# Kernel optimization log

Measured on AMD Instinct MI355X. Metric: run time of the kernel, lower is better.

## Reference

```python
import jax, jax.numpy as jnp
import numpy as np

# EXP-HYDRO concrete realization of HydrologyModel.
# Parameter order matches _parameter_bounds key order; bounds per standard EXP-HYDRO.
PARAM_BOUNDS = [
    ("f",    0.0,  0.1),
    ("Smax", 100.0, 1500.0),
    ("Qmax", 10.0, 50.0),
    ("Df",   0.0,  5.0),
    ("Tmax", 0.0,  3.0),
    ("Tmin", -3.0, 0.0),
]
NEARZERO = 1e-6
T_STEPS = 1024
N_BASINS = 8192
N_PARAMS = len(PARAM_BOUNDS)


def _denormalize(static_params_norm):
    # sigmoid activation then affine map to bounds; returns dict name -> [B]
    act = jax.nn.sigmoid(static_params_norm)  # [B, P]
    return {name: lo + (hi - lo) * act[:, i]
            for i, (name, lo, hi) in enumerate(PARAM_BOUNDS)}


def _run_core(prcp, temp, pet, params, nearzero=NEARZERO):
    # prcp/temp/pet: [T, B]; params: dict of [B]
    f, Smax, Qmax = params["f"], params["Smax"], params["Qmax"]
    Df, Tmax, Tmin = params["Df"], params["Tmax"], params["Tmin"]

    def step(states, forc_t):
        snowpack, soilwater = states
        prcp_t, temp_t, pet_t = forc_t
        # hydroflux formulas (elementwise over basins)
        snowfall = jnp.where(temp_t < Tmin, prcp_t, 0.0)
        rainfall = prcp_t - snowfall
        melt = jnp.minimum(snowpack, Df * jnp.maximum(temp_t - Tmax, 0.0))
        evap = pet_t * jnp.minimum(soilwater / Smax, 1.0)
        baseflow = Qmax * jnp.exp(-f * jnp.maximum(Smax - soilwater, 0.0))
        surfaceflow = jnp.maximum(soilwater - Smax, 0.0)
        # stateflux formulas (state changes)
        d_snow = snowfall - melt
        d_soil = rainfall + melt - evap - baseflow - surfaceflow
        # state update with clamp(min=nearzero)
        new_snow = jnp.maximum(snowpack + d_snow, nearzero)
        new_soil = jnp.maximum(soilwater + d_soil, nearzero)
        out = jnp.stack([snowfall, rainfall, melt, evap,
                         baseflow, surfaceflow, d_snow, d_soil])  # [8, B]
        return (new_snow, new_soil), out

    B = prcp.shape[1]
    init = (jnp.zeros((B,), prcp.dtype), jnp.zeros((B,), prcp.dtype))
    _, outs = jax.lax.scan(step, init, (prcp, temp, pet))
    return outs  # [T, 8, B]


def setup_inputs() -> dict:
    key = jax.random.key(0)
    k1, k2, k3, k4 = jax.random.split(key, 4)
    prcp = jax.random.uniform(k1, (T_STEPS, N_BASINS), jnp.float32) * 10.0  # mm/day
    temp = jax.random.normal(k2, (T_STEPS, N_BASINS), jnp.float32) * 5.0    # deg C
    pet = jax.random.uniform(k3, (T_STEPS, N_BASINS), jnp.float32) * 5.0    # mm/day
    static_params_norm = jax.random.normal(k4, (N_BASINS, N_PARAMS), jnp.float32)
    return {"prcp": prcp, "temp": temp, "pet": pet,
            "static_params_norm": static_params_norm}


def reference(prcp, temp, pet, static_params_norm):
    params = _denormalize(static_params_norm)
    return _run_core(prcp, temp, pet, params)  # [T, 8, B]
```

## Files before the change

kernel.cpp:

```cpp
#include <hip/hip_runtime.h>

#define T_STEPS 1024
#define NB 8192
#define OUT_TSTRIDE (8 * NB)

__device__ __forceinline__ float sigmoidf_(float x) {
    return 1.0f / (1.0f + __expf(-x));
}

#define STEP(PR, TM, PE, TI)                                                   \
    do {                                                                       \
        float snowfall    = ((TM) < Tmin) ? (PR) : 0.0f;                       \
        float rainfall    = (PR) - snowfall;                                   \
        float melt        = fminf(snow, Df * fmaxf((TM) - Tmax, 0.0f));        \
        float evap        = (PE) * fminf(soil * rSmax, 1.0f);                  \
        float baseflow    = Qmax * __expf(nf * fmaxf(Smax - soil, 0.0f));      \
        float surfaceflow = fmaxf(soil - Smax, 0.0f);                          \
        float d_snow      = snowfall - melt;                                   \
        float d_soil = (((rainfall + melt) - evap) - baseflow) - surfaceflow;  \
        snow = fmaxf(snow + d_snow, 1e-6f);                                    \
        soil = fmaxf(soil + d_soil, 1e-6f);                                    \
        float sv;                                                              \
        if (CH == 0)      sv = snowfall;                                       \
        else if (CH == 1) sv = rainfall;                                       \
        else if (CH == 2) sv = melt;                                           \
        else if (CH == 3) sv = evap;                                           \
        else if (CH == 4) sv = baseflow;                                       \
        else if (CH == 5) sv = surfaceflow;                                    \
        else if (CH == 6) sv = d_snow;                                         \
        else              sv = d_soil;                                         \
        op[(size_t)(TI) * OUT_TSTRIDE] = sv;                                   \
    } while (0)

template <int CH>
__device__ __forceinline__ void run_basin(const float* __restrict__ pp,
                                          const float* __restrict__ tp,
                                          const float* __restrict__ ep,
                                          float* __restrict__ op, float f,
                                          float Smax, float Qmax, float Df,
                                          float Tmax, float Tmin) {
    const float rSmax = 1.0f / Smax;
    const float nf    = -f;
    float snow = 0.0f, soil = 0.0f;

    float Pa[8], Ta[8], Ea[8], Pb[8], Tb[8], Eb[8];
#pragma unroll
    for (int i = 0; i < 8; ++i) {
        Pa[i] = pp[i * NB];
        Ta[i] = tp[i * NB];
        Ea[i] = ep[i * NB];
    }
#pragma unroll
    for (int i = 0; i < 8; ++i) {
        Pb[i] = pp[(8 + i) * NB];
        Tb[i] = tp[(8 + i) * NB];
        Eb[i] = ep[(8 + i) * NB];
    }

    for (int tb = 0; tb < T_STEPS; tb += 16) {
#pragma unroll
        for (int i = 0; i < 8; ++i) STEP(Pa[i], Ta[i], Ea[i], tb + i);
#pragma unroll
        for (int i = 0; i < 8; ++i) {
            int t2 = tb + 16 + i;
            t2     = (t2 > T_STEPS - 1) ? (T_STEPS - 1) : t2;
            Pa[i]  = pp[t2 * NB];
            Ta[i]  = tp[t2 * NB];
            Ea[i]  = ep[t2 * NB];
        }
#pragma unroll
        for (int i = 0; i < 8; ++i) STEP(Pb[i], Tb[i], Eb[i], tb + 8 + i);
#pragma unroll
        for (int i = 0; i < 8; ++i) {
            int t2 = tb + 24 + i;
            t2     = (t2 > T_STEPS - 1) ? (T_STEPS - 1) : t2;
            Pb[i]  = pp[t2 * NB];
            Tb[i]  = tp[t2 * NB];
            Eb[i]  = ep[t2 * NB];
        }
    }
}

extern "C" __global__ void __launch_bounds__(256, 1)
    hydro_kernel(const float* __restrict__ prcp, const float* __restrict__ temp,
                 const float* __restrict__ pet, const float* __restrict__ spn,
                 float* __restrict__ out) {
    const int lane  = threadIdx.x & 63;
    const int wav   = threadIdx.x >> 6;
    const int h     = blockIdx.x & 1;
    const int g     = blockIdx.x >> 1;
    const int basin = g * 64 + lane;
    const int ch    = h * 4 + wav;

    const float* p6  = spn + basin * 6;
    const float f    = 0.1f * sigmoidf_(p6[0]);
    const float Smax = 100.0f + 1400.0f * sigmoidf_(p6[1]);
    const float Qmax = 10.0f + 40.0f * sigmoidf_(p6[2]);
    const float Df   = 5.0f * sigmoidf_(p6[3]);
    const float Tmax = 3.0f * sigmoidf_(p6[4]);
    const float Tmin = -3.0f + 3.0f * sigmoidf_(p6[5]);

    const float* pp = prcp + basin;
    const float* tp = temp + basin;
    const float* ep = pet + basin;
    float* op       = out + (size_t)ch * NB + basin;

    switch (__builtin_amdgcn_readfirstlane(ch)) {
        case 0: run_basin<0>(pp, tp, ep, op, f, Smax, Qmax, Df, Tmax, Tmin); break;
        case 1: run_basin<1>(pp, tp, ep, op, f, Smax, Qmax, Df, Tmax, Tmin); break;
        case 2: run_basin<2>(pp, tp, ep, op, f, Smax, Qmax, Df, Tmax, Tmin); break;
        case 3: run_basin<3>(pp, tp, ep, op, f, Smax, Qmax, Df, Tmax, Tmin); break;
        case 4: run_basin<4>(pp, tp, ep, op, f, Smax, Qmax, Df, Tmax, Tmin); break;
        case 5: run_basin<5>(pp, tp, ep, op, f, Smax, Qmax, Df, Tmax, Tmin); break;
        case 6: run_basin<6>(pp, tp, ep, op, f, Smax, Qmax, Df, Tmax, Tmin); break;
        default: run_basin<7>(pp, tp, ep, op, f, Smax, Qmax, Df, Tmax, Tmin); break;
    }
}

extern "C" void kernel_launch(void* const* d_in, const int* in_sizes, int n_in,
                              void* d_out, int out_size, void* d_ws,
                              size_t ws_size, hipStream_t stream) {
    const float* prcp = (const float*)d_in[0];
    const float* temp = (const float*)d_in[1];
    const float* pet  = (const float*)d_in[2];
    const float* spn  = (const float*)d_in[3];
    float* out        = (float*)d_out;

    hydro_kernel<<<dim3(256), dim3(256), 0, stream>>>(prcp, temp, pet, spn, out);
}
```

Baseline: 405.9 us.

## Split time into segments with prefix recompute and two channels per wave

Each wave now stores two output channels instead of one, halving the redundant recurrence evaluation per basin. The time axis is split into four 256-step segments across more blocks, and each block replays the prefix of the recurrence without stores to rebuild its starting state. This increases the number of resident blocks and cuts total arithmetic, at the cost of uneven per-block work and larger register arrays for deeper prefetch.

Result: slower. 435.2 us (+7.2%).

```diff
diff --git a/kernel.cpp b/kernel.cpp
--- a/kernel.cpp
+++ b/kernel.cpp
@@ -8,89 +8,124 @@
     return 1.0f / (1.0f + __expf(-x));
 }
 
-#define STEP(PR, TM, PE, TI)                                                   \
+#define CORE(PR, TM, PE)                                                       \
+    float snowfall    = ((TM) < Tmin) ? (PR) : 0.0f;                           \
+    float rainfall    = (PR) - snowfall;                                       \
+    float melt        = fminf(snow, Df * fmaxf((TM) - Tmax, 0.0f));            \
+    float evap        = (PE) * fminf(soil * rSmax, 1.0f);                      \
+    float baseflow    = Qmax * __expf(nf * fmaxf(Smax - soil, 0.0f));          \
+    float surfaceflow = fmaxf(soil - Smax, 0.0f);                              \
+    float d_snow      = snowfall - melt;                                       \
+    float d_soil = (((rainfall + melt) - evap) - baseflow) - surfaceflow;      \
+    snow = fmaxf(snow + d_snow, 1e-6f);                                        \
+    soil = fmaxf(soil + d_soil, 1e-6f);
+
+#define STEP_NS(PR, TM, PE)                                                    \
     do {                                                                       \
-        float snowfall    = ((TM) < Tmin) ? (PR) : 0.0f;                       \
-        float rainfall    = (PR) - snowfall;                                   \
-        float melt        = fminf(snow, Df * fmaxf((TM) - Tmax, 0.0f));        \
-        float evap        = (PE) * fminf(soil * rSmax, 1.0f);                  \
-        float baseflow    = Qmax * __expf(nf * fmaxf(Smax - soil, 0.0f));      \
-        float surfaceflow = fmaxf(soil - Smax, 0.0f);                          \
-        float d_snow      = snowfall - melt;                                   \
-        float d_soil = (((rainfall + melt) - evap) - baseflow) - surfaceflow;  \
-        snow = fmaxf(snow + d_snow, 1e-6f);                                    \
-        soil = fmaxf(soil + d_soil, 1e-6f);                                    \
-        float sv;                                                              \
-        if (CH == 0)      sv = snowfall;                                       \
-        else if (CH == 1) sv = rainfall;                                       \
-        else if (CH == 2) sv = melt;                                           \
-        else if (CH == 3) sv = evap;                                           \
-        else if (CH == 4) sv = baseflow;                                       \
-        else if (CH == 5) sv = surfaceflow;                                    \
-        else if (CH == 6) sv = d_snow;                                         \
-        else              sv = d_soil;                                         \
-        op[(size_t)(TI) * OUT_TSTRIDE] = sv;                                   \
+        CORE(PR, TM, PE)                                                       \
+        (void)rainfall; (void)evap; (void)baseflow; (void)surfaceflow;         \
+        (void)d_snow; (void)d_soil;                                            \
     } while (0)
 
-template <int CH>
+#define STEP_ST(PR, TM, PE)                                                    \
+    do {                                                                       \
+        CORE(PR, TM, PE)                                                       \
+        float sv0, sv1;                                                        \
+        if (CP == 0)      { sv0 = snowfall; sv1 = rainfall; }                  \
+        else if (CP == 1) { sv0 = melt;     sv1 = evap; }                      \
+        else if (CP == 2) { sv0 = baseflow; sv1 = surfaceflow; }               \
+        else              { sv0 = d_snow;   sv1 = d_soil; }                    \
+        op[0]  = sv0;                                                          \
+        op[NB] = sv1;                                                          \
+        op += OUT_TSTRIDE;                                                     \
+    } while (0)
+
+template <int CP>
 __device__ __forceinline__ void run_basin(const float* __restrict__ pp,
                                           const float* __restrict__ tp,
                                           const float* __restrict__ ep,
                                           float* __restrict__ op, float f,
                                           float Smax, float Qmax, float Df,
-                                          float Tmax, float Tmin) {
+                                          float Tmax, float Tmin,
+                                          int segStart) {
     const float rSmax = 1.0f / Smax;
     const float nf    = -f;
     float snow = 0.0f, soil = 0.0f;
 
-    float Pa[8], Ta[8], Ea[8], Pb[8], Tb[8], Eb[8];
+    float Pa[16], Ta[16], Ea[16], Pb[16], Tb[16], Eb[16];
+
+    if (segStart > 0) {
 #pragma unroll
-    for (int i = 0; i < 8; ++i) {
-        Pa[i] = pp[i * NB];
-        Ta[i] = tp[i * NB];
-        Ea[i] = ep[i * NB];
+        for (int i = 0; i < 16; ++i) {
+            Pa[i] = pp[i * NB]; Ta[i] = tp[i * NB]; Ea[i] = ep[i * NB];
+        }
+#pragma unroll
+        for (int i = 0; i < 16; ++i) {
+            Pb[i] = pp[(16 + i) * NB]; Tb[i] = tp[(16 + i) * NB];
+            Eb[i] = ep[(16 + i) * NB];
+        }
+        for (int tb = 0; tb < segStart; tb += 32) {
+#pragma unroll
+            for (int i = 0; i < 16; ++i) STEP_NS(Pa[i], Ta[i], Ea[i]);
+#pragma unroll
+            for (int i = 0; i < 16; ++i) {
+                int t2 = tb + 32 + i;
+                Pa[i] = pp[t2 * NB]; Ta[i] = tp[t2 * NB]; Ea[i] = ep[t2 * NB];
+            }
+#pragma unroll
+            for (int i = 0; i < 16; ++i) STEP_NS(Pb[i], Tb[i], Eb[i]);
+#pragma unroll
+            for (int i = 0; i < 16; ++i) {
+                int t2 = tb + 48 + i;
+                Pb[i] = pp[t2 * NB]; Tb[i] = tp[t2 * NB]; Eb[i] = ep[t2 * NB];
+            }
+        }
+    }
+
+#pragma unroll
+    for (int i = 0; i < 16; ++i) {
+        int t = segStart + i;
+        Pa[i] = pp[t * NB]; Ta[i] = tp[t * NB]; Ea[i] = ep[t * NB];
     }
 #pragma unroll
-    for (int i = 0; i < 8; ++i) {
-        Pb[i] = pp[(8 + i) * NB];
-        Tb[i] = tp[(8 + i) * NB];
-        Eb[i] = ep[(8 + i) * NB];
+    for (int i = 0; i < 16; ++i) {
+        int t = segStart + 16 + i;
+        Pb[i] = pp[t * NB]; Tb[i] = tp[t * NB]; Eb[i] = ep[t * NB];
     }
-
-    for (int tb = 0; tb < T_STEPS; tb += 16) {
+    for (int tb = segStart; tb < segStart + 256; tb += 32) {
 #pragma unroll
-        for (int i = 0; i < 8; ++i) STEP(Pa[i], Ta[i], Ea[i], tb + i);
+        for (int i = 0; i < 16; ++i) STEP_ST(Pa[i], Ta[i], Ea[i]);
 #pragma unroll
-        for (int i = 0; i < 8; ++i) {
-            int t2 = tb + 16 + i;
-            t2     = (t2 > T_STEPS - 1) ? (T_STEPS - 1) : t2;
-            Pa[i]  = pp[t2 * NB];
-            Ta[i]  = tp[t2 * NB];
-            Ea[i]  = ep[t2 * NB];
+        for (int i = 0; i < 16; ++i) {
+            int t2 = tb + 32 + i;
+            t2 = (t2 > T_STEPS - 1) ? (T_STEPS - 1) : t2;
+            Pa[i] = pp[t2 * NB]; Ta[i] = tp[t2 * NB]; Ea[i] = ep[t2 * NB];
         }
 #pragma unroll
-        for (int i = 0; i < 8; ++i) STEP(Pb[i], Tb[i], Eb[i], tb + 8 + i);
+        for (int i = 0; i < 16; ++i) STEP_ST(Pb[i], Tb[i], Eb[i]);
 #pragma unroll
-        for (int i = 0; i < 8; ++i) {
-            int t2 = tb + 24 + i;
-            t2     = (t2 > T_STEPS - 1) ? (T_STEPS - 1) : t2;
-            Pb[i]  = pp[t2 * NB];
-            Tb[i]  = tp[t2 * NB];
-            Eb[i]  = ep[t2 * NB];
+        for (int i = 0; i < 16; ++i) {
+            int t2 = tb + 48 + i;
+            t2 = (t2 > T_STEPS - 1) ? (T_STEPS - 1) : t2;
+            Pb[i] = pp[t2 * NB]; Tb[i] = tp[t2 * NB]; Eb[i] = ep[t2 * NB];
         }
     }
 }
 
-extern "C" __global__ void __launch_bounds__(256, 1)
+extern "C" __global__ void __launch_bounds__(256, 2)
     hydro_kernel(const float* __restrict__ prcp, const float* __restrict__ temp,
                  const float* __restrict__ pet, const float* __restrict__ spn,
                  float* __restrict__ out) {
     const int lane  = threadIdx.x & 63;
-    const int wav   = threadIdx.x >> 6;
-    const int h     = blockIdx.x & 1;
-    const int g     = blockIdx.x >> 1;
-    const int basin = g * 64 + lane;
-    const int ch    = h * 4 + wav;
+    const int w     = threadIdx.x >> 6;
+    const int b     = blockIdx.x;
+    const int x     = b & 7;
+    const int r     = b >> 3;
+    const int seg   = r & 3;
+    const int gg    = r >> 2;
+    const int group = gg * 8 + x;
+    const int basin = group * 64 + lane;
+    const int segStart = seg << 8;
 
     const float* p6  = spn + basin * 6;
     const float f    = 0.1f * sigmoidf_(p6[0]);
@@ -103,17 +138,13 @@
     const float* pp = prcp + basin;
     const float* tp = temp + basin;
     const float* ep = pet + basin;
-    float* op       = out + (size_t)ch * NB + basin;
+    float* op = out + (size_t)segStart * OUT_TSTRIDE + (size_t)(2 * w) * NB + basin;
 
-    switch (__builtin_amdgcn_readfirstlane(ch)) {
-        case 0: run_basin<0>(pp, tp, ep, op, f, Smax, Qmax, Df, Tmax, Tmin); break;
-        case 1: run_basin<1>(pp, tp, ep, op, f, Smax, Qmax, Df, Tmax, Tmin); break;
-        case 2: run_basin<2>(pp, tp, ep, op, f, Smax, Qmax, Df, Tmax, Tmin); break;
-        case 3: run_basin<3>(pp, tp, ep, op, f, Smax, Qmax, Df, Tmax, Tmin); break;
-        case 4: run_basin<4>(pp, tp, ep, op, f, Smax, Qmax, Df, Tmax, Tmin); break;
-        case 5: run_basin<5>(pp, tp, ep, op, f, Smax, Qmax, Df, Tmax, Tmin); break;
-        case 6: run_basin<6>(pp, tp, ep, op, f, Smax, Qmax, Df, Tmax, Tmin); break;
-        default: run_basin<7>(pp, tp, ep, op, f, Smax, Qmax, Df, Tmax, Tmin); break;
+    switch (__builtin_amdgcn_readfirstlane(w)) {
+        case 0:  run_basin<0>(pp, tp, ep, op, f, Smax, Qmax, Df, Tmax, Tmin, segStart); break;
+        case 1:  run_basin<1>(pp, tp, ep, op, f, Smax, Qmax, Df, Tmax, Tmin, segStart); break;
+        case 2:  run_basin<2>(pp, tp, ep, op, f, Smax, Qmax, Df, Tmax, Tmin, segStart); break;
+        default: run_basin<3>(pp, tp, ep, op, f, Smax, Qmax, Df, Tmax, Tmin, segStart); break;
     }
 }
 
@@ -126,5 +157,5 @@
     const float* spn  = (const float*)d_in[3];
     float* out        = (float*)d_out;
 
-    hydro_kernel<<<dim3(256), dim3(256), 0, stream>>>(prcp, temp, pet, spn, out);
+    hydro_kernel<<<dim3(512), dim3(256), 0, stream>>>(prcp, temp, pet, spn, out);
 }
```

## Stage forcings in LDS via async loads, two channels per wave, split store ranges

Applied to the files above, without the earlier changes.

Forcing tiles of 32 timesteps are copied into double-buffered LDS with global_load_lds, so the four waves of a block share one load instead of each reading global memory separately. Each wave now emits two output channels instead of one. Two block types are paired per basin group: both run the recurrence from the start, and each stores a different range of output tiles so store work is split evenly. The cost is redundant recurrence computation, since one block type re-runs 24 to 32 tiles, plus a block-wide barrier on every tile.

New measurement: 372.5 us. 1.09x faster.

```diff
diff --git a/kernel.cpp b/kernel.cpp
--- a/kernel.cpp
+++ b/kernel.cpp
@@ -1,83 +1,89 @@
 #include <hip/hip_runtime.h>
+#include <stdint.h>
 
-#define T_STEPS 1024
 #define NB 8192
 #define OUT_TSTRIDE (8 * NB)
+#define TILE 32
+#define LDS_F 6144
 
 __device__ __forceinline__ float sigmoidf_(float x) {
     return 1.0f / (1.0f + __expf(-x));
 }
 
-#define STEP(PR, TM, PE, TI)                                                   \
-    do {                                                                       \
-        float snowfall    = ((TM) < Tmin) ? (PR) : 0.0f;                       \
-        float rainfall    = (PR) - snowfall;                                   \
-        float melt        = fminf(snow, Df * fmaxf((TM) - Tmax, 0.0f));        \
-        float evap        = (PE) * fminf(soil * rSmax, 1.0f);                  \
-        float baseflow    = Qmax * __expf(nf * fmaxf(Smax - soil, 0.0f));      \
-        float surfaceflow = fmaxf(soil - Smax, 0.0f);                          \
-        float d_snow      = snowfall - melt;                                   \
-        float d_soil = (((rainfall + melt) - evap) - baseflow) - surfaceflow;  \
-        snow = fmaxf(snow + d_snow, 1e-6f);                                    \
-        soil = fmaxf(soil + d_soil, 1e-6f);                                    \
-        float sv;                                                              \
-        if (CH == 0)      sv = snowfall;                                       \
-        else if (CH == 1) sv = rainfall;                                       \
-        else if (CH == 2) sv = melt;                                           \
-        else if (CH == 3) sv = evap;                                           \
-        else if (CH == 4) sv = baseflow;                                       \
-        else if (CH == 5) sv = surfaceflow;                                    \
-        else if (CH == 6) sv = d_snow;                                         \
-        else              sv = d_soil;                                         \
-        op[(size_t)(TI) * OUT_TSTRIDE] = sv;                                   \
-    } while (0)
+__device__ __forceinline__ void async16(const float* g, float* l) {
+    __builtin_amdgcn_global_load_lds(
+        (const __attribute__((address_space(1))) void*)g,
+        (__attribute__((address_space(3))) void*)l, 16, 0, 0);
+}
 
-template <int CH>
-__device__ __forceinline__ void run_basin(const float* __restrict__ pp,
-                                          const float* __restrict__ tp,
-                                          const float* __restrict__ ep,
-                                          float* __restrict__ op, float f,
-                                          float Smax, float Qmax, float Df,
-                                          float Tmax, float Tmin) {
+__device__ __forceinline__ void fill_tile(const float* __restrict__ prcp,
+                                          const float* __restrict__ temp,
+                                          const float* __restrict__ pet,
+                                          float* lds, int t0, int tid,
+                                          int gbase) {
+#pragma unroll
+    for (int r = 0; r < 6; ++r) {
+        const float* src = (r < 2) ? prcp : ((r < 4) ? temp : pet);
+        int tt = ((r & 1) << 4) + (tid >> 4);
+        int t  = t0 + tt;
+        t      = (t > 1023) ? 1023 : t;
+        const float* g = src + (size_t)t * NB + gbase + ((tid & 15) << 2);
+        float* l       = lds + (r << 10) + (tid << 2);
+        async16(g, l);
+    }
+}
+
+template <int CP>
+__device__ void run(const float* __restrict__ prcp,
+                    const float* __restrict__ temp,
+                    const float* __restrict__ pet, float* __restrict__ out,
+                    float (*lds)[LDS_F], int tid, int lane, int gbase,
+                    int basin, int ntiles, int lo1, int hi1, int lo2, float f,
+                    float Smax, float Qmax, float Df, float Tmax, float Tmin) {
     const float rSmax = 1.0f / Smax;
     const float nf    = -f;
     float snow = 0.0f, soil = 0.0f;
+    float* const outBase = out + (size_t)(2 * CP) * NB + basin;
 
-    float Pa[8], Ta[8], Ea[8], Pb[8], Tb[8], Eb[8];
+    fill_tile(prcp, temp, pet, lds[0], 0, tid, gbase);
+    __syncthreads();
+
+    for (int tile = 0; tile < ntiles; ++tile) {
+        const int cur = tile & 1;
+        fill_tile(prcp, temp, pet, lds[cur ^ 1], (tile + 1) * TILE, tid, gbase);
+
+        const bool doStore = (tile >= lo1 && tile < hi1) || (tile >= lo2);
+        const float* lp    = lds[cur];
+        float* o = outBase + (size_t)tile * TILE * OUT_TSTRIDE;
 #pragma unroll
-    for (int i = 0; i < 8; ++i) {
-        Pa[i] = pp[i * NB];
-        Ta[i] = tp[i * NB];
-        Ea[i] = ep[i * NB];
-    }
-#pragma unroll
-    for (int i = 0; i < 8; ++i) {
-        Pb[i] = pp[(8 + i) * NB];
-        Tb[i] = tp[(8 + i) * NB];
-        Eb[i] = ep[(8 + i) * NB];
-    }
+        for (int i = 0; i < TILE; ++i) {
+            const float P  = lp[i * 64 + lane];
+            const float Tm = lp[2048 + i * 64 + lane];
+            const float Pe = lp[4096 + i * 64 + lane];
 
-    for (int tb = 0; tb < T_STEPS; tb += 16) {
-#pragma unroll
-        for (int i = 0; i < 8; ++i) STEP(Pa[i], Ta[i], Ea[i], tb + i);
-#pragma unroll
-        for (int i = 0; i < 8; ++i) {
-            int t2 = tb + 16 + i;
-            t2     = (t2 > T_STEPS - 1) ? (T_STEPS - 1) : t2;
-            Pa[i]  = pp[t2 * NB];
-            Ta[i]  = tp[t2 * NB];
-            Ea[i]  = ep[t2 * NB];
+            const float snowfall    = (Tm < Tmin) ? P : 0.0f;
+            const float rainfall    = P - snowfall;
+            const float melt        = fminf(snow, Df * fmaxf(Tm - Tmax, 0.0f));
+            const float evap        = Pe * fminf(soil * rSmax, 1.0f);
+            const float baseflow    = Qmax * __expf(nf * fmaxf(Smax - soil, 0.0f));
+            const float surfaceflow = fmaxf(soil - Smax, 0.0f);
+            const float d_snow      = snowfall - melt;
+            const float d_soil =
+                (((rainfall + melt) - evap) - baseflow) - surfaceflow;
+            snow = fmaxf(snow + d_snow, 1e-6f);
+            soil = fmaxf(soil + d_soil, 1e-6f);
+
+            if (doStore) {
+                float sv0, sv1;
+                if (CP == 0)      { sv0 = snowfall; sv1 = rainfall; }
+                else if (CP == 1) { sv0 = melt;     sv1 = evap; }
+                else if (CP == 2) { sv0 = baseflow; sv1 = surfaceflow; }
+                else              { sv0 = d_snow;   sv1 = d_soil; }
+                o[(size_t)i * OUT_TSTRIDE]      = sv0;
+                o[(size_t)i * OUT_TSTRIDE + NB] = sv1;
+            }
         }
-#pragma unroll
-        for (int i = 0; i < 8; ++i) STEP(Pb[i], Tb[i], Eb[i], tb + 8 + i);
-#pragma unroll
-        for (int i = 0; i < 8; ++i) {
-            int t2 = tb + 24 + i;
-            t2     = (t2 > T_STEPS - 1) ? (T_STEPS - 1) : t2;
-            Pb[i]  = pp[t2 * NB];
-            Tb[i]  = tp[t2 * NB];
-            Eb[i]  = ep[t2 * NB];
-        }
+        __syncthreads();
     }
 }
 
@@ -85,12 +91,21 @@
     hydro_kernel(const float* __restrict__ prcp, const float* __restrict__ temp,
                  const float* __restrict__ pet, const float* __restrict__ spn,
                  float* __restrict__ out) {
-    const int lane  = threadIdx.x & 63;
-    const int wav   = threadIdx.x >> 6;
-    const int h     = blockIdx.x & 1;
-    const int g     = blockIdx.x >> 1;
-    const int basin = g * 64 + lane;
-    const int ch    = h * 4 + wav;
+    __shared__ float lds[2][LDS_F];
+
+    const int tid   = threadIdx.x;
+    const int lane  = tid & 63;
+    const int w     = tid >> 6;
+    const int b     = blockIdx.x;
+    const int group = (b >> 4) * 8 + (b & 7);
+    const int type  = (b >> 3) & 1;
+    const int gbase = group * 64;
+    const int basin = gbase + lane;
+
+    const int ntiles = type ? 24 : 32;
+    const int lo1    = type ? 8 : 0;
+    const int hi1    = type ? 24 : 8;
+    const int lo2    = type ? 999 : 24;
 
     const float* p6  = spn + basin * 6;
     const float f    = 0.1f * sigmoidf_(p6[0]);
@@ -100,20 +115,23 @@
     const float Tmax = 3.0f * sigmoidf_(p6[4]);
     const float Tmin = -3.0f + 3.0f * sigmoidf_(p6[5]);
 
-    const float* pp = prcp + basin;
-    const float* tp = temp + basin;
-    const float* ep = pet + basin;
-    float* op       = out + (size_t)ch * NB + basin;
-
-    switch (__builtin_amdgcn_readfirstlane(ch)) {
-        case 0: run_basin<0>(pp, tp, ep, op, f, Smax, Qmax, Df, Tmax, Tmin); break;
-        case 1: run_basin<1>(pp, tp, ep, op, f, Smax, Qmax, Df, Tmax, Tmin); break;
-        case 2: run_basin<2>(pp, tp, ep, op, f, Smax, Qmax, Df, Tmax, Tmin); break;
-        case 3: run_basin<3>(pp, tp, ep, op, f, Smax, Qmax, Df, Tmax, Tmin); break;
-        case 4: run_basin<4>(pp, tp, ep, op, f, Smax, Qmax, Df, Tmax, Tmin); break;
-        case 5: run_basin<5>(pp, tp, ep, op, f, Smax, Qmax, Df, Tmax, Tmin); break;
-        case 6: run_basin<6>(pp, tp, ep, op, f, Smax, Qmax, Df, Tmax, Tmin); break;
-        default: run_basin<7>(pp, tp, ep, op, f, Smax, Qmax, Df, Tmax, Tmin); break;
+    switch (__builtin_amdgcn_readfirstlane(w)) {
+        case 0:
+            run<0>(prcp, temp, pet, out, lds, tid, lane, gbase, basin, ntiles,
+                   lo1, hi1, lo2, f, Smax, Qmax, Df, Tmax, Tmin);
+            break;
+        case 1:
+            run<1>(prcp, temp, pet, out, lds, tid, lane, gbase, basin, ntiles,
+                   lo1, hi1, lo2, f, Smax, Qmax, Df, Tmax, Tmin);
+            break;
+        case 2:
+            run<2>(prcp, temp, pet, out, lds, tid, lane, gbase, basin, ntiles,
+                   lo1, hi1, lo2, f, Smax, Qmax, Df, Tmax, Tmin);
+            break;
+        default:
+            run<3>(prcp, temp, pet, out, lds, tid, lane, gbase, basin, ntiles,
+                   lo1, hi1, lo2, f, Smax, Qmax, Df, Tmax, Tmin);
+            break;
     }
 }
 
```
